# Optimization experiments

Hardware: AMD Instinct MI355X
Metric: run time of the kernel (lower is better)

Reference implementation:

```python
import jax, jax.numpy as jnp
import numpy as np

EMBED_DIM = 1024
NHEAD = 16
HEAD_DIM = EMBED_DIM // NHEAD  # 64
B, S = 2, 2048


def _rotate_half(x):
    x1, x2 = jnp.split(x, 2, axis=-1)
    return jnp.concatenate([-x2, x1], axis=-1)


def _apply_rope(t, cos, sin):
    # t: (B, H, S, Dh); cos/sin: (S, Dh) broadcast over leading dims
    return t * cos + _rotate_half(t) * sin


def setup_inputs() -> dict:
    key = jax.random.key(0)
    ks = jax.random.split(key, 6)
    x = jax.random.normal(ks[0], (B, S, EMBED_DIM), dtype=jnp.float32)
    # real RoPE tables: theta_i = 10000^(-2i/Dh), duplicated for the two halves
    inv_freq = 1.0 / (10000.0 ** (jnp.arange(0, HEAD_DIM, 2, dtype=jnp.float32) / HEAD_DIM))
    freqs = jnp.outer(jnp.arange(S, dtype=jnp.float32), inv_freq)  # (S, Dh/2)
    emb = jnp.concatenate([freqs, freqs], axis=-1)  # (S, Dh)
    cos = jnp.cos(emb)
    sin = jnp.sin(emb)
    W_in = jax.random.normal(ks[1], (EMBED_DIM, 3 * EMBED_DIM), dtype=jnp.float32) * 0.02
    b_in = jax.random.normal(ks[2], (3 * EMBED_DIM,), dtype=jnp.float32) * 0.02
    W_out = jax.random.normal(ks[3], (EMBED_DIM, EMBED_DIM), dtype=jnp.float32) * 0.02
    b_out = jax.random.normal(ks[4], (EMBED_DIM,), dtype=jnp.float32) * 0.02
    return {"x": x, "cos": cos, "sin": sin, "W_in": W_in, "b_in": b_in,
            "W_out": W_out, "b_out": b_out}


def reference(x, cos, sin, W_in, b_in, W_out, b_out):
    Bs, Ss, D = x.shape
    qkv = x @ W_in + b_in  # (B, S, 3D)
    q, k, v = jnp.split(qkv, 3, axis=-1)
    # (B, S, D) -> (B, H, S, Dh)
    def heads(t):
        return t.reshape(Bs, Ss, NHEAD, HEAD_DIM).transpose(0, 2, 1, 3)
    q, k, v = heads(q), heads(k), heads(v)
    q = _apply_rope(q, cos, sin)
    k = _apply_rope(k, cos, sin)
    scale = 1.0 / jnp.sqrt(jnp.array(HEAD_DIM, dtype=x.dtype))
    scores = jnp.einsum('bhqd,bhkd->bhqk', q, k) * scale
    attn = jax.nn.softmax(scores, axis=-1)
    out = jnp.einsum('bhqk,bhkd->bhqd', attn, v)
    out = out.transpose(0, 2, 1, 3).reshape(Bs, Ss, D)
    return out @ W_out + b_out
```

## Files before the change

kernel.cpp:

```cpp
#include <hip/hip_runtime.h>
#include <hip/hip_bf16.h>

typedef float f32x4 __attribute__((ext_vector_type(4)));
typedef short s16x8 __attribute__((ext_vector_type(8)));
typedef short s16x4 __attribute__((ext_vector_type(4)));

typedef const __attribute__((address_space(1))) unsigned int* as1u;
typedef __attribute__((address_space(3))) unsigned int* as3u;

__device__ __forceinline__ unsigned short f2bf(float f) {
    union { float f; unsigned u; } v; v.f = f;
    unsigned u = v.u;
    u += 0x7fffu + ((u >> 16) & 1u);
    return (unsigned short)(u >> 16);
}

__device__ __forceinline__ void gload16(const void* g, void* l3) {
    __builtin_amdgcn_global_load_lds((as1u)g, (as3u)l3, 16, 0, 0);
}

__device__ __forceinline__ int swzo(int row, int cb) {
    return row * 128 + (cb ^ ((row & 7) << 4));
}

#define LOG2E 1.4426950408889634f
#define QSCALE (0.125f * LOG2E)

__global__ __launch_bounds__(256) void xbf_kernel(
    const float* __restrict__ x, unsigned short* __restrict__ xb)
{
    size_t i = ((size_t)blockIdx.x * 256 + threadIdx.x) * 8;
    float4 a = *(const float4*)&x[i];
    float4 b = *(const float4*)&x[i + 4];
    s16x8 p;
    p[0] = (short)f2bf(a.x); p[1] = (short)f2bf(a.y);
    p[2] = (short)f2bf(a.z); p[3] = (short)f2bf(a.w);
    p[4] = (short)f2bf(b.x); p[5] = (short)f2bf(b.y);
    p[6] = (short)f2bf(b.z); p[7] = (short)f2bf(b.w);
    *(s16x8*)&xb[i] = p;
}

__global__ __launch_bounds__(256) void convT_kernel(
    const float* __restrict__ W, unsigned short* __restrict__ Wt, int K, int N)
{
    __shared__ alignas(16) short T[64 * 64];
    const int t = threadIdx.x;
    const int KB = K >> 6;
    const int kb = blockIdx.x % KB, nb = blockIdx.x / KB;
#pragma unroll
    for (int pass = 0; pass < 4; ++pass) {
        int k = pass * 16 + (t >> 4);
        int n4 = (t & 15) * 4;
        float4 v = *(const float4*)&W[(size_t)(kb * 64 + k) * N + nb * 64 + n4];
        short4 s4;
        s4.x = (short)f2bf(v.x); s4.y = (short)f2bf(v.y);
        s4.z = (short)f2bf(v.z); s4.w = (short)f2bf(v.w);
        *(short4*)((char*)T + k * 128 + ((n4 * 2) ^ ((k & 7) << 4))) = s4;
    }
    __syncthreads();
#pragma unroll
    for (int pass = 0; pass < 4; ++pass) {
        int n = pass * 16 + (t >> 4);
        int k4 = (t & 15) * 4;
        short4 s4;
        s4.x = *(const short*)((const char*)T + (k4 + 0) * 128 + ((n * 2) ^ (((k4 + 0) & 7) << 4)));
        s4.y = *(const short*)((const char*)T + (k4 + 1) * 128 + ((n * 2) ^ (((k4 + 1) & 7) << 4)));
        s4.z = *(const short*)((const char*)T + (k4 + 2) * 128 + ((n * 2) ^ (((k4 + 2) & 7) << 4)));
        s4.w = *(const short*)((const char*)T + (k4 + 3) * 128 + ((n * 2) ^ (((k4 + 3) & 7) << 4)));
        *(short4*)&Wt[(size_t)(nb * 64 + n) * K + kb * 64 + k4] = s4;
    }
}

__global__ __launch_bounds__(256) void qkv_rope_kernel(
    const unsigned short* __restrict__ xb, const unsigned short* __restrict__ Wt,
    const float* __restrict__ bias, const float* __restrict__ cosb,
    const float* __restrict__ sinb,
    unsigned short* __restrict__ Qb, unsigned short* __restrict__ Kb,
    unsigned short* __restrict__ Vb)
{
    __shared__ alignas(16) short As[128 * 64];
    __shared__ alignas(16) short Bs[128 * 64];
    const int bid = blockIdx.x;
    const int mb = bid & 31, nb = bid >> 5;
    const int t = threadIdx.x, w = t >> 6, l = t & 63;
    const int g = l >> 4, j = l & 15;
    const int wm = w >> 1, wn = w & 1;
    const int m0 = mb * 128, n0 = nb * 128;

    f32x4 acc[4][4];
#pragma unroll
    for (int mi = 0; mi < 4; ++mi)
#pragma unroll
        for (int ni = 0; ni < 4; ++ni) acc[mi][ni] = (f32x4){0.f, 0.f, 0.f, 0.f};

    for (int kt = 0; kt < 1024; kt += 64) {
#pragma unroll
        for (int i = 0; i < 4; ++i) {
            int pos = (w * 4 + i) * 1024 + l * 16;
            int r = pos >> 7;
            int lb = (pos & 127) ^ ((r & 7) << 4);
            gload16(&Wt[(size_t)(n0 + r) * 1024 + kt + (lb >> 1)],
                    (char*)Bs + (w * 4 + i) * 1024);
            gload16(&xb[(size_t)(m0 + r) * 1024 + kt + (lb >> 1)],
                    (char*)As + (w * 4 + i) * 1024);
        }
        __syncthreads();
#pragma unroll
        for (int kf = 0; kf < 2; ++kf) {
            s16x8 af[4], bv[4];
#pragma unroll
            for (int mi = 0; mi < 4; ++mi)
                af[mi] = *(const s16x8*)((const char*)As + swzo(wm * 64 + mi * 16 + j, kf * 64 + g * 16));
#pragma unroll
            for (int ni = 0; ni < 4; ++ni)
                bv[ni] = *(const s16x8*)((const char*)Bs + swzo(wn * 64 + ni * 16 + j, kf * 64 + g * 16));
#pragma unroll
            for (int mi = 0; mi < 4; ++mi)
#pragma unroll
                for (int ni = 0; ni < 4; ++ni)
                    acc[mi][ni] = __builtin_amdgcn_mfma_f32_16x16x32_bf16(af[mi], bv[ni], acc[mi][ni], 0, 0, 0);
        }
        __syncthreads();
    }

    const int row0 = m0 + wm * 64;
    const int col0 = n0 + wn * 64;
    const int sec = col0 >> 10;
    const int h = (col0 & 1023) >> 6;

    if (sec < 2) {
        unsigned short* dst = (sec == 0) ? Qb : Kb;
        const float qs = (sec == 0) ? QSCALE : 1.0f;
#pragma unroll
        for (int nt = 0; nt < 2; ++nt) {
            const int d = nt * 16 + j;
            const float b1 = bias[col0 + d];
            const float b2 = bias[col0 + d + 32];
#pragma unroll
            for (int mi = 0; mi < 4; ++mi) {
#pragma unroll
                for (int r = 0; r < 4; ++r) {
                    int row = row0 + mi * 16 + g * 4 + r;
                    int s = row & 2047, bb = row >> 11;
                    float c = cosb[s * 64 + d], sn = sinb[s * 64 + d];
                    float x1 = acc[mi][nt][r] + b1;
                    float x2 = acc[mi][nt + 2][r] + b2;
                    float lo = (x1 * c - x2 * sn) * qs;
                    float hi = (x1 * sn + x2 * c) * qs;
                    size_t base = ((size_t)(bb * 16 + h) * 2048 + s) * 64;
                    dst[base + d] = f2bf(lo);
                    dst[base + d + 32] = f2bf(hi);
                }
            }
        }
    } else {
#pragma unroll
        for (int nt = 0; nt < 4; ++nt) {
            const int d = nt * 16 + j;
            const float bvv = bias[col0 + d];
#pragma unroll
            for (int mi = 0; mi < 4; ++mi) {
#pragma unroll
                for (int r = 0; r < 4; ++r) {
                    int row = row0 + mi * 16 + g * 4 + r;
                    int s = row & 2047, bb = row >> 11;
                    size_t base = ((size_t)(bb * 16 + h) * 2048 + s) * 64;
                    Vb[base + d] = f2bf(acc[mi][nt][r] + bvv);
                }
            }
        }
    }
}

#define NTILES 32
__global__ __launch_bounds__(512) void attn_kernel(
    const unsigned short* __restrict__ Qb, const unsigned short* __restrict__ Kb,
    const unsigned short* __restrict__ Vb, unsigned short* __restrict__ AO)
{
    __shared__ alignas(16) short Ks[2][64 * 64];
    __shared__ alignas(16) short Vt[2][64 * 64];
    const int bid = blockIdx.x;
    const int qt = bid & 15, bh = bid >> 4;
    const int t = threadIdx.x, w = t >> 6, l = t & 63;
    const int g = l >> 4, j = l & 15;
    const bool godd = (g & 1);
    const unsigned short* Qh = Qb + (size_t)bh * 131072;
    const unsigned short* Kh = Kb + (size_t)bh * 131072;
    const unsigned short* Vh = Vb + (size_t)bh * 131072;
    const int q0 = qt * 128 + w * 16;

    s16x8 aq[2];
    aq[0] = *(const s16x8*)&Qh[(size_t)(q0 + j) * 64 + g * 8];
    aq[1] = *(const s16x8*)&Qh[(size_t)(q0 + j) * 64 + 32 + g * 8];

    float lt_ = 0.f;
    f32x4 o[4];
#pragma unroll
    for (int dt = 0; dt < 4; ++dt) o[dt] = (f32x4){0.f, 0.f, 0.f, 0.f};

    const bool vrole = (w < 4);
    const int tv = t & 255;
    const int vk = (tv & 31) * 2;
    const int vd = (tv >> 5) * 8;
    const int kw = (w & 3);

    s16x8 va, vb2;
    if (vrole) {
        va  = *(const s16x8*)&Vh[(size_t)vk * 64 + vd];
        vb2 = *(const s16x8*)&Vh[(size_t)(vk + 1) * 64 + vd];
    } else {
#pragma unroll
        for (int i = 0; i < 2; ++i) {
            int pos = (kw * 2 + i) * 1024 + l * 16;
            int r = pos >> 7, lb = (pos & 127) ^ ((r & 7) << 4);
            gload16(&Kh[(size_t)r * 64 + (lb >> 1)], (char*)Ks[0] + (kw * 2 + i) * 1024);
        }
    }
    asm volatile("s_waitcnt vmcnt(0)" ::: "memory");
    if (vrole) {
#pragma unroll
        for (int dd = 0; dd < 8; ++dd) {
            int d = vd + dd;
            unsigned pkv = (unsigned)(unsigned short)va[dd] | ((unsigned)(unsigned short)vb2[dd] << 16);
            *(unsigned*)((char*)Vt[0] + d * 128 + ((vk * 2) ^ ((d & 7) << 4))) = pkv;
        }
    }
    asm volatile("s_waitcnt lgkmcnt(0)" ::: "memory");
    __builtin_amdgcn_s_barrier();

    for (int tt = 0; tt < NTILES; ++tt) {
        const int cur = tt & 1, nxt = cur ^ 1;
        const int kvp = ((tt + 1) & (NTILES - 1)) * 64;

        if (vrole) {
            va  = *(const s16x8*)&Vh[(size_t)(kvp + vk) * 64 + vd];
            vb2 = *(const s16x8*)&Vh[(size_t)(kvp + vk + 1) * 64 + vd];
        } else {
#pragma unroll
            for (int i = 0; i < 2; ++i) {
                int pos = (kw * 2 + i) * 1024 + l * 16;
                int r = pos >> 7, lb = (pos & 127) ^ ((r & 7) << 4);
                gload16(&Kh[(size_t)(kvp + r) * 64 + (lb >> 1)], (char*)Ks[nxt] + (kw * 2 + i) * 1024);
            }
        }

        f32x4 sc[4];
#pragma unroll
        for (int nt = 0; nt < 4; ++nt) sc[nt] = (f32x4){0.f, 0.f, 0.f, 0.f};
        __builtin_amdgcn_s_setprio(1);
#pragma unroll
        for (int kf = 0; kf < 2; ++kf) {
            s16x8 bk[4];
#pragma unroll
            for (int nt = 0; nt < 4; ++nt)
                bk[nt] = *(const s16x8*)((const char*)Ks[cur] + swzo(nt * 16 + j, kf * 64 + g * 16));
#pragma unroll
            for (int nt = 0; nt < 4; ++nt)
                sc[nt] = __builtin_amdgcn_mfma_f32_16x16x32_bf16(bk[nt], aq[kf], sc[nt], 0, 0, 0);
        }
        __builtin_amdgcn_s_setprio(0);

        float rs = 0.f;
#pragma unroll
        for (int nt = 0; nt < 4; ++nt)
#pragma unroll
            for (int r = 0; r < 4; ++r) {
                sc[nt][r] = __builtin_amdgcn_exp2f(sc[nt][r]);
                rs += sc[nt][r];
            }
        lt_ += rs;

        unsigned pk[4][2];
#pragma unroll
        for (int nt = 0; nt < 4; ++nt)
#pragma unroll
            for (int s = 0; s < 2; ++s)
                asm("v_cvt_pk_bf16_f32 %0, %1, %2"
                    : "=v"(pk[nt][s]) : "v"(sc[nt][2 * s]), "v"(sc[nt][2 * s + 1]));

#pragma unroll
        for (int kf = 0; kf < 2; ++kf) {
            unsigned A0 = pk[2 * kf][0], A1 = pk[2 * kf][1];
            unsigned B0 = pk[2 * kf + 1][0], B1 = pk[2 * kf + 1][1];
            asm("v_permlane32_swap_b32 %0, %1" : "+v"(A0), "+v"(B0));
            asm("v_permlane32_swap_b32 %0, %1" : "+v"(A1), "+v"(B1));
            unsigned tB0 = __shfl_xor((int)B0, 16), tA0 = __shfl_xor((int)A0, 16);
            unsigned tB1 = __shfl_xor((int)B1, 16), tA1 = __shfl_xor((int)A1, 16);
            union { unsigned u[4]; s16x8 v; } fr;
            fr.u[0] = godd ? tB0 : A0;
            fr.u[1] = godd ? tB1 : A1;
            fr.u[2] = godd ? B0 : tA0;
            fr.u[3] = godd ? B1 : tA1;
            __builtin_amdgcn_s_setprio(1);
#pragma unroll
            for (int dt = 0; dt < 4; ++dt) {
                s16x8 vb = *(const s16x8*)((const char*)Vt[cur] + swzo(dt * 16 + j, kf * 64 + g * 16));
                o[dt] = __builtin_amdgcn_mfma_f32_16x16x32_bf16(fr.v, vb, o[dt], 0, 0, 0);
            }
            __builtin_amdgcn_s_setprio(0);
        }

        if (vrole) {
#pragma unroll
            for (int dd = 0; dd < 8; ++dd) {
                int d = vd + dd;
                unsigned pkv = (unsigned)(unsigned short)va[dd] | ((unsigned)(unsigned short)vb2[dd] << 16);
                *(unsigned*)((char*)Vt[nxt] + d * 128 + ((vk * 2) ^ ((d & 7) << 4))) = pkv;
            }
        }
        asm volatile("s_waitcnt vmcnt(0) lgkmcnt(0)" ::: "memory");
        __builtin_amdgcn_s_barrier();
    }

    lt_ += __shfl_xor(lt_, 16);
    lt_ += __shfl_xor(lt_, 32);

    const int b = bh >> 4, h = bh & 15;
#pragma unroll
    for (int r = 0; r < 4; ++r) {
        float inv = 1.0f / __shfl(lt_, g * 4 + r);
        int s = q0 + g * 4 + r;
        size_t base = ((size_t)b * 2048 + s) * 1024 + h * 64;
#pragma unroll
        for (int dt = 0; dt < 4; ++dt)
            AO[base + dt * 16 + j] = f2bf(o[dt][r] * inv);
    }
}

__global__ __launch_bounds__(256) void out_gemm_kernel(
    const unsigned short* __restrict__ A, const unsigned short* __restrict__ Wot,
    const float* __restrict__ bias, float* __restrict__ out)
{
    __shared__ alignas(16) short As[128 * 64];
    __shared__ alignas(16) short Bs[128 * 64];
    const int bid = blockIdx.x;
    const int mb = bid & 31, nb = bid >> 5;
    const int t = threadIdx.x, w = t >> 6, l = t & 63;
    const int g = l >> 4, j = l & 15;
    const int wm = w >> 1, wn = w & 1;
    const int m0 = mb * 128, n0 = nb * 128;

    f32x4 acc[4][4];
#pragma unroll
    for (int mi = 0; mi < 4; ++mi)
#pragma unroll
        for (int ni = 0; ni < 4; ++ni) acc[mi][ni] = (f32x4){0.f, 0.f, 0.f, 0.f};

    for (int kt = 0; kt < 1024; kt += 64) {
#pragma unroll
        for (int i = 0; i < 4; ++i) {
            int pos = (w * 4 + i) * 1024 + l * 16;
            int r = pos >> 7;
            int lb = (pos & 127) ^ ((r & 7) << 4);
            gload16(&A[(size_t)(m0 + r) * 1024 + kt + (lb >> 1)],
                    (char*)As + (w * 4 + i) * 1024);
            gload16(&Wot[(size_t)(n0 + r) * 1024 + kt + (lb >> 1)],
                    (char*)Bs + (w * 4 + i) * 1024);
        }
        __syncthreads();
#pragma unroll
        for (int kf = 0; kf < 2; ++kf) {
            s16x8 af[4], bv[4];
#pragma unroll
            for (int mi = 0; mi < 4; ++mi)
                af[mi] = *(const s16x8*)((const char*)As + swzo(wm * 64 + mi * 16 + j, kf * 64 + g * 16));
#pragma unroll
            for (int ni = 0; ni < 4; ++ni)
                bv[ni] = *(const s16x8*)((const char*)Bs + swzo(wn * 64 + ni * 16 + j, kf * 64 + g * 16));
#pragma unroll
            for (int mi = 0; mi < 4; ++mi)
#pragma unroll
                for (int ni = 0; ni < 4; ++ni)
                    acc[mi][ni] = __builtin_amdgcn_mfma_f32_16x16x32_bf16(af[mi], bv[ni], acc[mi][ni], 0, 0, 0);
        }
        __syncthreads();
    }

    const int row0 = m0 + wm * 64;
    const int col0 = n0 + wn * 64;
#pragma unroll
    for (int ni = 0; ni < 4; ++ni) {
        const int col = col0 + ni * 16 + j;
        const float bvv = bias[col];
#pragma unroll
        for (int mi = 0; mi < 4; ++mi)
#pragma unroll
            for (int r = 0; r < 4; ++r) {
                int row = row0 + mi * 16 + g * 4 + r;
                out[(size_t)row * 1024 + col] = acc[mi][ni][r] + bvv;
            }
    }
}

extern "C" void kernel_launch(void* const* d_in, const int* in_sizes, int n_in,
                              void* d_out, int out_size, void* d_ws, size_t ws_size,
                              hipStream_t stream) {
    const float* x     = (const float*)d_in[0];
    const float* cosb  = (const float*)d_in[1];
    const float* sinb  = (const float*)d_in[2];
    const float* W_in  = (const float*)d_in[3];
    const float* b_in  = (const float*)d_in[4];
    const float* W_out = (const float*)d_in[5];
    const float* b_out = (const float*)d_in[6];
    float* out = (float*)d_out;

    const size_t HBUF = 2ull * 16 * 2048 * 64;
    if (ws_size < 4 * HBUF * sizeof(unsigned short)) return;
    unsigned short* Qb = (unsigned short*)d_ws;
    unsigned short* Kb = Qb + HBUF;
    unsigned short* Vb = Kb + HBUF;
    unsigned short* R  = Vb + HBUF;
    unsigned short* Wt_in = R;
    unsigned short* AO    = R;
    unsigned short* Wot   = Qb;
    unsigned short* xbuf  = (unsigned short*)d_out;

    hipLaunchKernelGGL(xbf_kernel, dim3(2048), dim3(256), 0, stream, x, xbuf);
    hipLaunchKernelGGL(convT_kernel, dim3(768), dim3(256), 0, stream,
                       W_in, Wt_in, 1024, 3072);
    hipLaunchKernelGGL(qkv_rope_kernel, dim3(768), dim3(256), 0, stream,
                       xbuf, Wt_in, b_in, cosb, sinb, Qb, Kb, Vb);
    hipLaunchKernelGGL(attn_kernel, dim3(512), dim3(512), 0, stream,
                       Qb, Kb, Vb, AO);
    hipLaunchKernelGGL(convT_kernel, dim3(256), dim3(256), 0, stream,
                       W_out, Wot, 1024, 1024);
    hipLaunchKernelGGL(out_gemm_kernel, dim3(256), dim3(256), 0, stream,
                       AO, Wot, b_out, out);
}
```

Baseline: 132.1 us.

## Load K fragments directly from global, split V transpose across all waves, remap blocks

Removes the shared-memory K staging buffer. Each wave now reads its K MFMA operands straight from global memory (relying on L1/L2 reuse across waves), and all 512 threads share the V transpose into LDS instead of splitting the block into V and K roles. The block index is remapped so that consecutive blocks cover different heads, and launch bounds now request 4 blocks per CU to raise occupancy. The trade-off is more global and cache traffic for K plus exposed global-load latency, since the K loads for the current tile are issued in the same iteration that consumes them.

```diff
diff --git a/kernel.cpp b/kernel.cpp
--- a/kernel.cpp
+++ b/kernel.cpp
@@ -173,14 +173,14 @@
 }
 
 #define NTILES 32
-__global__ __launch_bounds__(512) void attn_kernel(
+__global__ __launch_bounds__(512, 4) void attn_kernel(
     const unsigned short* __restrict__ Qb, const unsigned short* __restrict__ Kb,
     const unsigned short* __restrict__ Vb, unsigned short* __restrict__ AO)
 {
-    __shared__ alignas(16) short Ks[2][64 * 64];
     __shared__ alignas(16) short Vt[2][64 * 64];
     const int bid = blockIdx.x;
-    const int qt = bid & 15, bh = bid >> 4;
+    const int bh = (bid & 7) + ((bid >> 7) << 3);
+    const int qt = (bid >> 3) & 15;
     const int t = threadIdx.x, w = t >> 6, l = t & 63;
     const int g = l >> 4, j = l & 15;
     const bool godd = (g & 1);
@@ -198,66 +198,44 @@
 #pragma unroll
     for (int dt = 0; dt < 4; ++dt) o[dt] = (f32x4){0.f, 0.f, 0.f, 0.f};
 
-    const bool vrole = (w < 4);
-    const int tv = t & 255;
-    const int vk = (tv & 31) * 2;
-    const int vd = (tv >> 5) * 8;
-    const int kw = (w & 3);
-
-    s16x8 va, vb2;
-    if (vrole) {
-        va  = *(const s16x8*)&Vh[(size_t)vk * 64 + vd];
-        vb2 = *(const s16x8*)&Vh[(size_t)(vk + 1) * 64 + vd];
-    } else {
-#pragma unroll
-        for (int i = 0; i < 2; ++i) {
-            int pos = (kw * 2 + i) * 1024 + l * 16;
-            int r = pos >> 7, lb = (pos & 127) ^ ((r & 7) << 4);
-            gload16(&Kh[(size_t)r * 64 + (lb >> 1)], (char*)Ks[0] + (kw * 2 + i) * 1024);
-        }
-    }
-    asm volatile("s_waitcnt vmcnt(0)" ::: "memory");
-    if (vrole) {
-#pragma unroll
-        for (int dd = 0; dd < 8; ++dd) {
-            int d = vd + dd;
-            unsigned pkv = (unsigned)(unsigned short)va[dd] | ((unsigned)(unsigned short)vb2[dd] << 16);
-            *(unsigned*)((char*)Vt[0] + d * 128 + ((vk * 2) ^ ((d & 7) << 4))) = pkv;
-        }
-    }
-    asm volatile("s_waitcnt lgkmcnt(0)" ::: "memory");
-    __builtin_amdgcn_s_barrier();
+    const int vk2 = (t & 31) * 2;
+    const int vd4 = ((t >> 5) & 15) * 4;
+
+    const int kfo = j * 64 + g * 8;
+
+    s16x4 va = *(const s16x4*)&Vh[(size_t)vk2 * 64 + vd4];
+    s16x4 vb2 = *(const s16x4*)&Vh[(size_t)(vk2 + 1) * 64 + vd4];
+#pragma unroll
+    for (int i = 0; i < 4; ++i) {
+        int d = vd4 + i;
+        unsigned pkv = (unsigned)(unsigned short)va[i] | ((unsigned)(unsigned short)vb2[i] << 16);
+        *(unsigned*)((char*)Vt[0] + d * 128 + ((vk2 * 2) ^ ((d & 7) << 4))) = pkv;
+    }
+    __syncthreads();
 
     for (int tt = 0; tt < NTILES; ++tt) {
         const int cur = tt & 1, nxt = cur ^ 1;
         const int kvp = ((tt + 1) & (NTILES - 1)) * 64;
 
-        if (vrole) {
-            va  = *(const s16x8*)&Vh[(size_t)(kvp + vk) * 64 + vd];
-            vb2 = *(const s16x8*)&Vh[(size_t)(kvp + vk + 1) * 64 + vd];
-        } else {
-#pragma unroll
-            for (int i = 0; i < 2; ++i) {
-                int pos = (kw * 2 + i) * 1024 + l * 16;
-                int r = pos >> 7, lb = (pos & 127) ^ ((r & 7) << 4);
-                gload16(&Kh[(size_t)(kvp + r) * 64 + (lb >> 1)], (char*)Ks[nxt] + (kw * 2 + i) * 1024);
-            }
-        }
-
+        va  = *(const s16x4*)&Vh[(size_t)(kvp + vk2) * 64 + vd4];
+        vb2 = *(const s16x4*)&Vh[(size_t)(kvp + vk2 + 1) * 64 + vd4];
+
+        const unsigned short* Kt = Kh + (size_t)(tt * 64) * 64;
+        s16x8 bk[2][4];
+#pragma unroll
+        for (int kf = 0; kf < 2; ++kf)
+#pragma unroll
+            for (int nt = 0; nt < 4; ++nt)
+                bk[kf][nt] = *(const s16x8*)&Kt[nt * 1024 + kf * 32 + kfo];
         f32x4 sc[4];
 #pragma unroll
         for (int nt = 0; nt < 4; ++nt) sc[nt] = (f32x4){0.f, 0.f, 0.f, 0.f};
         __builtin_amdgcn_s_setprio(1);
 #pragma unroll
-        for (int kf = 0; kf < 2; ++kf) {
-            s16x8 bk[4];
+        for (int kf = 0; kf < 2; ++kf)
 #pragma unroll
             for (int nt = 0; nt < 4; ++nt)
-                bk[nt] = *(const s16x8*)((const char*)Ks[cur] + swzo(nt * 16 + j, kf * 64 + g * 16));
-#pragma unroll
-            for (int nt = 0; nt < 4; ++nt)
-                sc[nt] = __builtin_amdgcn_mfma_f32_16x16x32_bf16(bk[nt], aq[kf], sc[nt], 0, 0, 0);
-        }
+                sc[nt] = __builtin_amdgcn_mfma_f32_16x16x32_bf16(bk[kf][nt], aq[kf], sc[nt], 0, 0, 0);
         __builtin_amdgcn_s_setprio(0);
 
         float rs = 0.f;
@@ -300,16 +278,13 @@
             __builtin_amdgcn_s_setprio(0);
         }
 
-        if (vrole) {
-#pragma unroll
-            for (int dd = 0; dd < 8; ++dd) {
-                int d = vd + dd;
-                unsigned pkv = (unsigned)(unsigned short)va[dd] | ((unsigned)(unsigned short)vb2[dd] << 16);
-                *(unsigned*)((char*)Vt[nxt] + d * 128 + ((vk * 2) ^ ((d & 7) << 4))) = pkv;
-            }
-        }
-        asm volatile("s_waitcnt vmcnt(0) lgkmcnt(0)" ::: "memory");
-        __builtin_amdgcn_s_barrier();
+#pragma unroll
+        for (int i = 0; i < 4; ++i) {
+            int d = vd4 + i;
+            unsigned pkv = (unsigned)(unsigned short)va[i] | ((unsigned)(unsigned short)vb2[i] << 16);
+            *(unsigned*)((char*)Vt[nxt] + d * 128 + ((vk2 * 2) ^ ((d & 7) << 4))) = pkv;
+        }
+        __syncthreads();
     }
 
     lt_ += __shfl_xor(lt_, 16);
```

Result: slower. 236.7 us (+79.1%).

## Process two KV tiles per barrier round and remap block-to-head order

Applied to the files above, without the earlier changes.

The attention loop now stages 128 keys/values per double-buffered round instead of 64, halving the number of block-wide barriers and waitcnt drains. It also adds a min-blocks hint to launch_bounds and reorders the block index so eight consecutive blocks cover different heads, which changes L2 locality of K/V reads. In exchange LDS use doubles to 64KB per block and more registers hold prefetched V, which may limit occupancy.

```diff
diff --git a/kernel.cpp b/kernel.cpp
--- a/kernel.cpp
+++ b/kernel.cpp
@@ -3,7 +3,6 @@
 
 typedef float f32x4 __attribute__((ext_vector_type(4)));
 typedef short s16x8 __attribute__((ext_vector_type(8)));
-typedef short s16x4 __attribute__((ext_vector_type(4)));
 
 typedef const __attribute__((address_space(1))) unsigned int* as1u;
 typedef __attribute__((address_space(3))) unsigned int* as3u;
@@ -172,15 +171,16 @@
     }
 }
 
-#define NTILES 32
-__global__ __launch_bounds__(512) void attn_kernel(
+#define NROUND 16
+__global__ __launch_bounds__(512, 4) void attn_kernel(
     const unsigned short* __restrict__ Qb, const unsigned short* __restrict__ Kb,
     const unsigned short* __restrict__ Vb, unsigned short* __restrict__ AO)
 {
-    __shared__ alignas(16) short Ks[2][64 * 64];
-    __shared__ alignas(16) short Vt[2][64 * 64];
+    __shared__ alignas(16) short Ks[2][2 * 64 * 64];
+    __shared__ alignas(16) short Vt[2][2 * 64 * 64];
     const int bid = blockIdx.x;
-    const int qt = bid & 15, bh = bid >> 4;
+    const int bh = (bid & 7) + ((bid >> 7) << 3);
+    const int qt = (bid >> 3) & 15;
     const int t = threadIdx.x, w = t >> 6, l = t & 63;
     const int g = l >> 4, j = l & 15;
     const bool godd = (g & 1);
@@ -204,109 +204,130 @@
     const int vd = (tv >> 5) * 8;
     const int kw = (w & 3);
 
-    s16x8 va, vb2;
+    s16x8 va[2], vb2[2];
+
     if (vrole) {
-        va  = *(const s16x8*)&Vh[(size_t)vk * 64 + vd];
-        vb2 = *(const s16x8*)&Vh[(size_t)(vk + 1) * 64 + vd];
+#pragma unroll
+        for (int s = 0; s < 2; ++s) {
+            va[s]  = *(const s16x8*)&Vh[(size_t)(s * 64 + vk) * 64 + vd];
+            vb2[s] = *(const s16x8*)&Vh[(size_t)(s * 64 + vk + 1) * 64 + vd];
+        }
     } else {
 #pragma unroll
-        for (int i = 0; i < 2; ++i) {
-            int pos = (kw * 2 + i) * 1024 + l * 16;
-            int r = pos >> 7, lb = (pos & 127) ^ ((r & 7) << 4);
-            gload16(&Kh[(size_t)r * 64 + (lb >> 1)], (char*)Ks[0] + (kw * 2 + i) * 1024);
+        for (int i = 0; i < 4; ++i) {
+            int p = (kw * 4 + i) * 1024 + l * 16;
+            int s = p >> 13, q = p & 8191;
+            int r = q >> 7, lb = (q & 127) ^ ((r & 7) << 4);
+            gload16(&Kh[(size_t)(s * 64 + r) * 64 + (lb >> 1)],
+                    (char*)Ks[0] + (kw * 4 + i) * 1024);
         }
     }
     asm volatile("s_waitcnt vmcnt(0)" ::: "memory");
     if (vrole) {
 #pragma unroll
-        for (int dd = 0; dd < 8; ++dd) {
-            int d = vd + dd;
-            unsigned pkv = (unsigned)(unsigned short)va[dd] | ((unsigned)(unsigned short)vb2[dd] << 16);
-            *(unsigned*)((char*)Vt[0] + d * 128 + ((vk * 2) ^ ((d & 7) << 4))) = pkv;
-        }
+        for (int s = 0; s < 2; ++s)
+#pragma unroll
+            for (int dd = 0; dd < 8; ++dd) {
+                int d = vd + dd;
+                unsigned pkv = (unsigned)(unsigned short)va[s][dd] | ((unsigned)(unsigned short)vb2[s][dd] << 16);
+                *(unsigned*)((char*)Vt[0] + s * 8192 + d * 128 + ((vk * 2) ^ ((d & 7) << 4))) = pkv;
+            }
     }
     asm volatile("s_waitcnt lgkmcnt(0)" ::: "memory");
     __builtin_amdgcn_s_barrier();
 
-    for (int tt = 0; tt < NTILES; ++tt) {
-        const int cur = tt & 1, nxt = cur ^ 1;
-        const int kvp = ((tt + 1) & (NTILES - 1)) * 64;
+    for (int rr = 0; rr < NROUND; ++rr) {
+        const int cur = rr & 1, nxt = cur ^ 1;
+        const int kvp = ((rr + 1) & (NROUND - 1)) * 128;
 
         if (vrole) {
-            va  = *(const s16x8*)&Vh[(size_t)(kvp + vk) * 64 + vd];
-            vb2 = *(const s16x8*)&Vh[(size_t)(kvp + vk + 1) * 64 + vd];
+#pragma unroll
+            for (int s = 0; s < 2; ++s) {
+                va[s]  = *(const s16x8*)&Vh[(size_t)(kvp + s * 64 + vk) * 64 + vd];
+                vb2[s] = *(const s16x8*)&Vh[(size_t)(kvp + s * 64 + vk + 1) * 64 + vd];
+            }
         } else {
 #pragma unroll
-            for (int i = 0; i < 2; ++i) {
-                int pos = (kw * 2 + i) * 1024 + l * 16;
-                int r = pos >> 7, lb = (pos & 127) ^ ((r & 7) << 4);
-                gload16(&Kh[(size_t)(kvp + r) * 64 + (lb >> 1)], (char*)Ks[nxt] + (kw * 2 + i) * 1024);
-            }
-        }
-
-        f32x4 sc[4];
-#pragma unroll
-        for (int nt = 0; nt < 4; ++nt) sc[nt] = (f32x4){0.f, 0.f, 0.f, 0.f};
-        __builtin_amdgcn_s_setprio(1);
-#pragma unroll
-        for (int kf = 0; kf < 2; ++kf) {
-            s16x8 bk[4];
+            for (int i = 0; i < 4; ++i) {
+                int p = (kw * 4 + i) * 1024 + l * 16;
+                int s = p >> 13, q = p & 8191;
+                int r = q >> 7, lb = (q & 127) ^ ((r & 7) << 4);
+                gload16(&Kh[(size_t)(kvp + s * 64 + r) * 64 + (lb >> 1)],
+                        (char*)Ks[nxt] + (kw * 4 + i) * 1024);
+            }
+        }
+
+#pragma unroll
+        for (int sub = 0; sub < 2; ++sub) {
+            const char* kbase = (const char*)Ks[cur] + sub * 8192;
+            const char* vbase = (const char*)Vt[cur] + sub * 8192;
+
+            f32x4 sc[4];
+#pragma unroll
+            for (int nt = 0; nt < 4; ++nt) sc[nt] = (f32x4){0.f, 0.f, 0.f, 0.f};
+            __builtin_amdgcn_s_setprio(1);
+#pragma unroll
+            for (int kf = 0; kf < 2; ++kf) {
+                s16x8 bk[4];
+#pragma unroll
+                for (int nt = 0; nt < 4; ++nt)
+                    bk[nt] = *(const s16x8*)(kbase + swzo(nt * 16 + j, kf * 64 + g * 16));
+#pragma unroll
+                for (int nt = 0; nt < 4; ++nt)
+                    sc[nt] = __builtin_amdgcn_mfma_f32_16x16x32_bf16(bk[nt], aq[kf], sc[nt], 0, 0, 0);
+            }
+            __builtin_amdgcn_s_setprio(0);
+
+            float rs = 0.f;
 #pragma unroll
             for (int nt = 0; nt < 4; ++nt)
-                bk[nt] = *(const s16x8*)((const char*)Ks[cur] + swzo(nt * 16 + j, kf * 64 + g * 16));
+#pragma unroll
+                for (int r = 0; r < 4; ++r) {
+                    sc[nt][r] = __builtin_amdgcn_exp2f(sc[nt][r]);
+                    rs += sc[nt][r];
+                }
+            lt_ += rs;
+
+            unsigned pk[4][2];
 #pragma unroll
             for (int nt = 0; nt < 4; ++nt)
-                sc[nt] = __builtin_amdgcn_mfma_f32_16x16x32_bf16(bk[nt], aq[kf], sc[nt], 0, 0, 0);
-        }
-        __builtin_amdgcn_s_setprio(0);
-
-        float rs = 0.f;
-#pragma unroll
-        for (int nt = 0; nt < 4; ++nt)
-#pragma unroll
-            for (int r = 0; r < 4; ++r) {
-                sc[nt][r] = __builtin_amdgcn_exp2f(sc[nt][r]);
-                rs += sc[nt][r];
-            }
-        lt_ += rs;
-
-        unsigned pk[4][2];
-#pragma unroll
-        for (int nt = 0; nt < 4; ++nt)
+#pragma unroll
+                for (int s = 0; s < 2; ++s)
+                    asm("v_cvt_pk_bf16_f32 %0, %1, %2"
+                        : "=v"(pk[nt][s]) : "v"(sc[nt][2 * s]), "v"(sc[nt][2 * s + 1]));
+
+#pragma unroll
+            for (int kf = 0; kf < 2; ++kf) {
+                unsigned A0 = pk[2 * kf][0], A1 = pk[2 * kf][1];
+                unsigned B0 = pk[2 * kf + 1][0], B1 = pk[2 * kf + 1][1];
+                asm("v_permlane32_swap_b32 %0, %1" : "+v"(A0), "+v"(B0));
+                asm("v_permlane32_swap_b32 %0, %1" : "+v"(A1), "+v"(B1));
+                unsigned tB0 = __shfl_xor((int)B0, 16), tA0 = __shfl_xor((int)A0, 16);
+                unsigned tB1 = __shfl_xor((int)B1, 16), tA1 = __shfl_xor((int)A1, 16);
+                union { unsigned u[4]; s16x8 v; } fr;
+                fr.u[0] = godd ? tB0 : A0;
+                fr.u[1] = godd ? tB1 : A1;
+                fr.u[2] = godd ? B0 : tA0;
+                fr.u[3] = godd ? B1 : tA1;
+                __builtin_amdgcn_s_setprio(1);
+#pragma unroll
+                for (int dt = 0; dt < 4; ++dt) {
+                    s16x8 vb = *(const s16x8*)(vbase + swzo(dt * 16 + j, kf * 64 + g * 16));
+                    o[dt] = __builtin_amdgcn_mfma_f32_16x16x32_bf16(fr.v, vb, o[dt], 0, 0, 0);
+                }
+                __builtin_amdgcn_s_setprio(0);
+            }
+        }
+
+        if (vrole) {
 #pragma unroll
             for (int s = 0; s < 2; ++s)
-                asm("v_cvt_pk_bf16_f32 %0, %1, %2"
-                    : "=v"(pk[nt][s]) : "v"(sc[nt][2 * s]), "v"(sc[nt][2 * s + 1]));
-
-#pragma unroll
-        for (int kf = 0; kf < 2; ++kf) {
-            unsigned A0 = pk[2 * kf][0], A1 = pk[2 * kf][1];
-            unsigned B0 = pk[2 * kf + 1][0], B1 = pk[2 * kf + 1][1];
-            asm("v_permlane32_swap_b32 %0, %1" : "+v"(A0), "+v"(B0));
-            asm("v_permlane32_swap_b32 %0, %1" : "+v"(A1), "+v"(B1));
-            unsigned tB0 = __shfl_xor((int)B0, 16), tA0 = __shfl_xor((int)A0, 16);
-            unsigned tB1 = __shfl_xor((int)B1, 16), tA1 = __shfl_xor((int)A1, 16);
-            union { unsigned u[4]; s16x8 v; } fr;
-            fr.u[0] = godd ? tB0 : A0;
-            fr.u[1] = godd ? tB1 : A1;
-            fr.u[2] = godd ? B0 : tA0;
-            fr.u[3] = godd ? B1 : tA1;
-            __builtin_amdgcn_s_setprio(1);
-#pragma unroll
-            for (int dt = 0; dt < 4; ++dt) {
-                s16x8 vb = *(const s16x8*)((const char*)Vt[cur] + swzo(dt * 16 + j, kf * 64 + g * 16));
-                o[dt] = __builtin_amdgcn_mfma_f32_16x16x32_bf16(fr.v, vb, o[dt], 0, 0, 0);
-            }
-            __builtin_amdgcn_s_setprio(0);
-        }
-
-        if (vrole) {
-#pragma unroll
-            for (int dd = 0; dd < 8; ++dd) {
-                int d = vd + dd;
-                unsigned pkv = (unsigned)(unsigned short)va[dd] | ((unsigned)(unsigned short)vb2[dd] << 16);
-                *(unsigned*)((char*)Vt[nxt] + d * 128 + ((vk * 2) ^ ((d & 7) << 4))) = pkv;
-            }
+#pragma unroll
+                for (int dd = 0; dd < 8; ++dd) {
+                    int d = vd + dd;
+                    unsigned pkv = (unsigned)(unsigned short)va[s][dd] | ((unsigned)(unsigned short)vb2[s][dd] << 16);
+                    *(unsigned*)((char*)Vt[nxt] + s * 8192 + d * 128 + ((vk * 2) ^ ((d & 7) << 4))) = pkv;
+                }
         }
         asm volatile("s_waitcnt vmcnt(0) lgkmcnt(0)" ::: "memory");
         __builtin_amdgcn_s_barrier();
```

Result: no change. 130.6 us (-1.1%).
